# Optimization experiments

Hardware: AMD Instinct MI355X
Metric: run time of the kernel (lower is better)

Reference implementation:

```python
import jax, jax.numpy as jnp
import numpy as np

PARENTS = np.array([-1, 0, 1, 1, 1])
NECK_CHAIN = np.array([1, 0])  # neck joint (1) up to root (0)
B, V, F, J, S, E = 512, 5023, 9976, 5, 100, 50
L_STAT, L_DYN, L_FULL, N_BUCKET = 51, 17, 68, 79


def rodrigues(rvec):
    """Axis-angle [N,3] -> rotation matrices [N,3,3]."""
    angle = jnp.linalg.norm(rvec + 1e-8, axis=-1, keepdims=True)  # [N,1]
    axis = rvec / angle
    s = jnp.sin(angle)[..., None]
    c = jnp.cos(angle)[..., None]
    rx, ry, rz = axis[:, 0], axis[:, 1], axis[:, 2]
    z = jnp.zeros_like(rx)
    K = jnp.stack([z, -rz, ry, rz, z, -rx, -ry, rx, z], axis=-1).reshape(-1, 3, 3)
    I = jnp.eye(3, dtype=rvec.dtype)
    return I + s * K + (1.0 - c) * (K @ K)


def verts2lmk(vertices, faces, lmk_faces_idx, lmk_bary):
    lmk_faces = faces[lmk_faces_idx]                               # [B,L,3]
    lmk_verts = jax.vmap(lambda v, f: v[f])(vertices, lmk_faces)   # [B,L,3verts,3xyz]
    return jnp.einsum('blfc,blf->blc', lmk_verts, lmk_bary)


def setup_inputs() -> dict:
    key = jax.random.key(0)
    ks = jax.random.split(key, 16)
    shape_params = jax.random.normal(ks[0], (B, S), jnp.float32)
    expression_params = jax.random.normal(ks[1], (B, E), jnp.float32)
    pose_params = 0.2 * jax.random.normal(ks[2], (B, 6), jnp.float32)
    eye_pose_params = 0.1 * jax.random.normal(ks[3], (B, 6), jnp.float32)
    v_template = jax.random.normal(ks[4], (V, 3), jnp.float32) * 0.1
    shapedirs = jax.random.normal(ks[5], (V, 3, S + E), jnp.float32) * 0.01
    posedirs = jax.random.normal(ks[6], ((J - 1) * 9, V * 3), jnp.float32) * 0.01
    jr = jax.random.uniform(ks[7], (J, V), jnp.float32)
    J_regressor = jr / jnp.sum(jr, axis=1, keepdims=True)
    lbs_weights = jax.nn.softmax(jax.random.normal(ks[8], (V, J), jnp.float32), axis=-1)
    faces = jax.random.randint(ks[9], (F, 3), 0, V)
    lmk_faces_idx = jax.random.randint(ks[10], (L_STAT,), 0, F)
    lb = jax.random.uniform(ks[11], (L_STAT, 3), jnp.float32) + 1e-3
    lmk_bary_coords = lb / jnp.sum(lb, axis=-1, keepdims=True)
    dynamic_lmk_faces_idx = jax.random.randint(ks[12], (N_BUCKET, L_DYN), 0, F)
    db = jax.random.uniform(ks[13], (N_BUCKET, L_DYN, 3), jnp.float32) + 1e-3
    dynamic_lmk_bary_coords = db / jnp.sum(db, axis=-1, keepdims=True)
    full_lmk_faces_idx = jax.random.randint(ks[14], (L_FULL,), 0, F)
    fb = jax.random.uniform(ks[15], (L_FULL, 3), jnp.float32) + 1e-3
    full_lmk_bary_coords = fb / jnp.sum(fb, axis=-1, keepdims=True)
    return {
        'shape_params': shape_params, 'expression_params': expression_params,
        'pose_params': pose_params, 'eye_pose_params': eye_pose_params,
        'v_template': v_template, 'shapedirs': shapedirs, 'posedirs': posedirs,
        'J_regressor': J_regressor, 'lbs_weights': lbs_weights, 'faces': faces,
        'lmk_faces_idx': lmk_faces_idx, 'lmk_bary_coords': lmk_bary_coords,
        'dynamic_lmk_faces_idx': dynamic_lmk_faces_idx,
        'dynamic_lmk_bary_coords': dynamic_lmk_bary_coords,
        'full_lmk_faces_idx': full_lmk_faces_idx,
        'full_lmk_bary_coords': full_lmk_bary_coords,
    }


def reference(shape_params, expression_params, pose_params, eye_pose_params,
              v_template, shapedirs, posedirs, J_regressor, lbs_weights, faces,
              lmk_faces_idx, lmk_bary_coords, dynamic_lmk_faces_idx,
              dynamic_lmk_bary_coords, full_lmk_faces_idx, full_lmk_bary_coords):
    b = shape_params.shape[0]
    nv = v_template.shape[0]
    dt = shape_params.dtype
    betas = jnp.concatenate([shape_params, expression_params], axis=1)          # [B,150]
    neck = jnp.zeros((b, 3), dtype=dt)
    full_pose = jnp.concatenate(
        [pose_params[:, :3], neck, pose_params[:, 3:], eye_pose_params], axis=1)  # [B,15]
    # shape + expression blendshapes
    v_shaped = v_template[None] + jnp.einsum('bl,vcl->bvc', betas, shapedirs)   # [B,V,3]
    joints = jnp.einsum('jv,bvc->bjc', J_regressor, v_shaped)                   # [B,5,3]
    rot_mats = rodrigues(full_pose.reshape(-1, 3)).reshape(b, J, 3, 3)          # [B,5,3,3]
    I3 = jnp.eye(3, dtype=dt)
    pose_feature = (rot_mats[:, 1:] - I3).reshape(b, -1)                        # [B,36]
    v_posed = v_shaped + (pose_feature @ posedirs).reshape(b, nv, 3)
    # kinematic chain -> global joint transforms
    rel_J = joints.at[:, 1:].add(-joints[:, PARENTS[1:]])
    tm = jnp.zeros((b, J, 4, 4), dtype=dt)
    tm = tm.at[:, :, :3, :3].set(rot_mats).at[:, :, :3, 3].set(rel_J).at[:, :, 3, 3].set(1.0)
    chain = [tm[:, 0]]
    for i in range(1, J):
        chain.append(chain[PARENTS[i]] @ tm[:, i])
    A = jnp.stack(chain, axis=1)                                                # [B,5,4,4]
    Rj = jnp.einsum('bjmn,bjn->bjm', A[:, :, :3, :3], joints)
    A_rel = A.at[:, :, :3, 3].add(-Rj)
    # per-vertex skinning
    T = jnp.einsum('vj,bjmn->bvmn', lbs_weights, A_rel)                         # [B,V,4,4]
    vertices = jnp.einsum('bvmn,bvn->bvm', T[:, :, :3, :3], v_posed) + T[:, :, :3, 3]
    # dynamic contour landmark selection from neck kin-chain relative rotation
    aa = full_pose.reshape(b, J, 3)[:, NECK_CHAIN]                              # [B,2,3]
    rc = rodrigues(aa.reshape(-1, 3)).reshape(b, len(NECK_CHAIN), 3, 3)
    rel_rot = jnp.broadcast_to(I3, (b, 3, 3))
    for idx in range(len(NECK_CHAIN)):
        rel_rot = rc[:, idx] @ rel_rot
    sy = jnp.sqrt(rel_rot[:, 0, 0] ** 2 + rel_rot[:, 1, 0] ** 2)
    y_deg = jnp.arctan2(-rel_rot[:, 2, 0], sy) * (180.0 / np.pi)
    y_rot = jnp.round(jnp.minimum(y_deg, 39.0)).astype(jnp.int32)
    neg_mask = y_rot < 0
    big_neg = y_rot < -39
    neg_vals = jnp.where(big_neg, 78, 39 - y_rot)
    y_rot = jnp.where(neg_mask, neg_vals, y_rot)                                # [B] in [0,79)
    dyn_faces = dynamic_lmk_faces_idx[y_rot]                                    # [B,17]
    dyn_bary = dynamic_lmk_bary_coords[y_rot]                                   # [B,17,3]
    lf = jnp.concatenate([dyn_faces, jnp.broadcast_to(lmk_faces_idx[None], (b, lmk_faces_idx.shape[0]))], axis=1)
    lb = jnp.concatenate([dyn_bary, jnp.broadcast_to(lmk_bary_coords[None], (b,) + lmk_bary_coords.shape)], axis=1)
    landmarks2d = verts2lmk(vertices, faces, lf, lb)
    ff = jnp.broadcast_to(full_lmk_faces_idx[None], (b, full_lmk_faces_idx.shape[0]))
    fb = jnp.broadcast_to(full_lmk_bary_coords[None], (b,) + full_lmk_bary_coords.shape)
    landmarks3d = verts2lmk(vertices, faces, ff, fb)
    return (vertices, landmarks2d, landmarks3d)
```

## Files before the change

kernel.cpp:

```cpp
#include <hip/hip_runtime.h>
#include <cstddef>
#include <cstdint>

#define cB   512
#define cV   5023
#define cS   100
#define cE   50
#define cJ   5
#define cLD  17
#define cLF  68

#define cV3    15069
#define cNPAD  15072
#define cKPAD  192

#define OUT_V  ((size_t)cB * cV * 3)
#define OUT_L  ((size_t)cB * cLF * 3)

#define WS_BTN   ((size_t)0)
#define WS_ATM   (WS_BTN + (size_t)cNPAD * 96)
#define WS_JS    (WS_ATM + (size_t)cB * 96)
#define WS_AREL  (WS_JS + 2272)
#define WS_PF    (WS_AREL + (size_t)cB * 60)
#define WS_YROT  (WS_PF + (size_t)cB * 36)

typedef __attribute__((ext_vector_type(8))) short short8;
typedef __attribute__((ext_vector_type(4))) float f32x4;

__device__ __forceinline__ unsigned short f2bf(float x) {
  unsigned int u = __float_as_uint(x);
  u = (u + 0x7fffu + ((u >> 16) & 1u)) >> 16;
  return (unsigned short)u;
}

__device__ __forceinline__ void rodrigues9(float rx, float ry, float rz, float* R) {
  float a0 = rx + 1e-8f, a1 = ry + 1e-8f, a2 = rz + 1e-8f;
  float angle = sqrtf(a0 * a0 + a1 * a1 + a2 * a2);
  float inv = 1.0f / angle;
  float x = rx * inv, y = ry * inv, z = rz * inv;
  float s = sinf(angle), c = cosf(angle);
  float t = 1.0f - c;
  float xy = x * y, xz = x * z, yz = y * z;
  R[0] = 1.0f - t * (y * y + z * z);
  R[1] = -s * z + t * xy;
  R[2] =  s * y + t * xz;
  R[3] =  s * z + t * xy;
  R[4] = 1.0f - t * (x * x + z * z);
  R[5] = -s * x + t * yz;
  R[6] = -s * y + t * xz;
  R[7] =  s * x + t * yz;
  R[8] = 1.0f - t * (x * x + y * y);
}

__global__ void k_js(const float* __restrict__ jreg, const float* __restrict__ sd,
                     const float* __restrict__ vt, float* __restrict__ JS) {
  int t = threadIdx.x;
  if (t >= 453) return;
  int c = t / 151, l = t - c * 151;
  int v0 = blockIdx.x * 32;
  int v1 = v0 + 32; if (v1 > cV) v1 = cV;
  float acc[5] = {0.f, 0.f, 0.f, 0.f, 0.f};
#pragma unroll 8
  for (int v = v0; v < v1; ++v) {
    float x = (l < 150) ? sd[(size_t)(v * 3 + c) * 150 + l] : vt[v * 3 + c];
#pragma unroll
    for (int j = 0; j < 5; ++j)
      acc[j] = fmaf(jreg[j * cV + v], x, acc[j]);
  }
#pragma unroll
  for (int j = 0; j < 5; ++j)
    atomicAdd(&JS[(j * 3 + c) * 151 + l], acc[j]);
}

__global__ __launch_bounds__(256) void k_batch(
    const float* __restrict__ shp, const float* __restrict__ expr,
    const float* __restrict__ pose, const float* __restrict__ eyep,
    const float* __restrict__ JSg, float* __restrict__ Arel,
    float* __restrict__ pf, int* __restrict__ yrot) {
  __shared__ float js[2272];
  __shared__ float sb[64 * 153];
  const int t = threadIdx.x;
  const int b0 = blockIdx.x * 64;
  for (int i = t; i < 2265; i += 256) js[i] = JSg[i];
  for (int e = t; e < 6400; e += 256) {
    int bl = e / 100, l = e - bl * 100;
    sb[bl * 153 + l] = shp[(size_t)(b0 + bl) * 100 + l];
  }
  for (int e = t; e < 3200; e += 256) {
    int bl = e / 50, l = e - bl * 50;
    sb[bl * 153 + 100 + l] = expr[(size_t)(b0 + bl) * 50 + l];
  }
  __syncthreads();
  if (t >= 64) return;
  int b = b0 + t;
  float jnt[5][3];
#pragma unroll
  for (int j = 0; j < 5; ++j)
#pragma unroll
    for (int c = 0; c < 3; ++c)
      jnt[j][c] = js[(j * 3 + c) * 151 + 150];
  for (int l = 0; l < 150; ++l) {
    float beta = sb[t * 153 + l];
#pragma unroll
    for (int j = 0; j < 5; ++j)
#pragma unroll
      for (int c = 0; c < 3; ++c)
        jnt[j][c] = fmaf(beta, js[(j * 3 + c) * 151 + l], jnt[j][c]);
  }
  float fp[5][3];
  fp[0][0] = pose[b * 6 + 0]; fp[0][1] = pose[b * 6 + 1]; fp[0][2] = pose[b * 6 + 2];
  fp[1][0] = 0.f; fp[1][1] = 0.f; fp[1][2] = 0.f;
  fp[2][0] = pose[b * 6 + 3]; fp[2][1] = pose[b * 6 + 4]; fp[2][2] = pose[b * 6 + 5];
  fp[3][0] = eyep[b * 6 + 0]; fp[3][1] = eyep[b * 6 + 1]; fp[3][2] = eyep[b * 6 + 2];
  fp[4][0] = eyep[b * 6 + 3]; fp[4][1] = eyep[b * 6 + 4]; fp[4][2] = eyep[b * 6 + 5];
  float R[5][9];
#pragma unroll
  for (int j = 0; j < 5; ++j) rodrigues9(fp[j][0], fp[j][1], fp[j][2], R[j]);
#pragma unroll
  for (int j = 1; j < 5; ++j)
#pragma unroll
    for (int r = 0; r < 9; ++r) {
      float id = (r == 0 || r == 4 || r == 8) ? 1.f : 0.f;
      pf[b * 36 + (j - 1) * 9 + r] = R[j][r] - id;
    }
  float rel[5][3];
#pragma unroll
  for (int c = 0; c < 3; ++c) {
    rel[0][c] = jnt[0][c];
    rel[1][c] = jnt[1][c] - jnt[0][c];
    rel[2][c] = jnt[2][c] - jnt[1][c];
    rel[3][c] = jnt[3][c] - jnt[1][c];
    rel[4][c] = jnt[4][c] - jnt[1][c];
  }
  float GR[5][9], Gt[5][3];
#pragma unroll
  for (int r = 0; r < 9; ++r) GR[0][r] = R[0][r];
#pragma unroll
  for (int c = 0; c < 3; ++c) Gt[0][c] = rel[0][c];
  const int par[5] = {0, 0, 1, 1, 1};
#pragma unroll
  for (int j = 1; j < 5; ++j) {
    int p = par[j];
#pragma unroll
    for (int r = 0; r < 3; ++r) {
#pragma unroll
      for (int cc = 0; cc < 3; ++cc)
        GR[j][r * 3 + cc] = GR[p][r * 3 + 0] * R[j][0 + cc] +
                            GR[p][r * 3 + 1] * R[j][3 + cc] +
                            GR[p][r * 3 + 2] * R[j][6 + cc];
      Gt[j][r] = Gt[p][r] + GR[p][r * 3 + 0] * rel[j][0] +
                            GR[p][r * 3 + 1] * rel[j][1] +
                            GR[p][r * 3 + 2] * rel[j][2];
    }
  }
#pragma unroll
  for (int j = 0; j < 5; ++j)
#pragma unroll
    for (int r = 0; r < 3; ++r) {
      float tj = Gt[j][r] - (GR[j][r * 3 + 0] * jnt[j][0] +
                             GR[j][r * 3 + 1] * jnt[j][1] +
                             GR[j][r * 3 + 2] * jnt[j][2]);
      Arel[b * 60 + j * 12 + r * 4 + 0] = GR[j][r * 3 + 0];
      Arel[b * 60 + j * 12 + r * 4 + 1] = GR[j][r * 3 + 1];
      Arel[b * 60 + j * 12 + r * 4 + 2] = GR[j][r * 3 + 2];
      Arel[b * 60 + j * 12 + r * 4 + 3] = tj;
    }
  float Ra[9], Rb[9];
  rodrigues9(fp[1][0], fp[1][1], fp[1][2], Ra);
  rodrigues9(fp[0][0], fp[0][1], fp[0][2], Rb);
  float r00 = Rb[0] * Ra[0] + Rb[1] * Ra[3] + Rb[2] * Ra[6];
  float r10 = Rb[3] * Ra[0] + Rb[4] * Ra[3] + Rb[5] * Ra[6];
  float r20 = Rb[6] * Ra[0] + Rb[7] * Ra[3] + Rb[8] * Ra[6];
  float sy = sqrtf(r00 * r00 + r10 * r10);
  float ydeg = atan2f(-r20, sy) * 57.29577951308232f;
  int y = (int)rintf(fminf(ydeg, 39.0f));
  if (y < 0) y = (y < -39) ? 78 : (39 - y);
  yrot[b] = y;
}

#define QB ((size_t)cNPAD * 48)
__global__ void k_prep(const float* __restrict__ sd, const float* __restrict__ shp,
                       const float* __restrict__ expr, const float* __restrict__ pfm,
                       unsigned int* __restrict__ btn_u2, unsigned int* __restrict__ atm_u2) {
  size_t idx = (size_t)blockIdx.x * 256 + threadIdx.x;
  unsigned short o[4];
  if (idx < QB) {
    int n = (int)(idx / 48), kq = (int)(idx - (size_t)n * 48);
#pragma unroll
    for (int j = 0; j < 4; ++j) {
      int k = kq * 4 + j;
      float v = (n < cV3 && k < 150) ? sd[(size_t)n * 150 + k] : 0.f;
      o[j] = f2bf(v);
    }
    btn_u2[idx * 2 + 0] = (unsigned int)o[0] | ((unsigned int)o[1] << 16);
    btn_u2[idx * 2 + 1] = (unsigned int)o[2] | ((unsigned int)o[3] << 16);
  } else {
    size_t r = idx - QB;
    int m = (int)(r / 48), kq = (int)(r - (size_t)m * 48);
#pragma unroll
    for (int j = 0; j < 4; ++j) {
      int k = kq * 4 + j;
      float v;
      if (k < cS)            v = shp[m * cS + k];
      else if (k < 150)      v = expr[m * cE + (k - cS)];
      else if (k < 186)      v = pfm[m * 36 + (k - 150)];
      else                   v = 0.f;
      o[j] = f2bf(v);
    }
    atm_u2[r * 2 + 0] = (unsigned int)o[0] | ((unsigned int)o[1] << 16);
    atm_u2[r * 2 + 1] = (unsigned int)o[2] | ((unsigned int)o[3] << 16);
  }
}

__global__ void k_pdT(const float* __restrict__ pd, unsigned int* __restrict__ btn_u) {
  __shared__ unsigned short T[64 * 36];
  const int t = threadIdx.x;
  const int n0 = blockIdx.x * 64;
#pragma unroll
  for (int it = 0; it < 9; ++it) {
    int e = t + it * 256;
    int kk = e >> 6, ln = e & 63;
    int n = n0 + ln;
    float v = (n < cV3) ? pd[(size_t)kk * cV3 + n] : 0.f;
    T[ln * 36 + kk] = f2bf(v);
  }
  __syncthreads();
  for (int e = t; e < 64 * 18; e += 256) {
    int ln = e / 18, d = e - ln * 18;
    int n = n0 + ln;
    if (n < cV3) {
      unsigned int w = (unsigned int)T[ln * 36 + 2 * d] |
                       ((unsigned int)T[ln * 36 + 2 * d + 1] << 16);
      btn_u[(size_t)n * 96 + 75 + d] = w;
    }
  }
}

__global__ __launch_bounds__(256, 4) void k_main(
    const unsigned short* __restrict__ BTn, const unsigned short* __restrict__ ATm,
    const float* __restrict__ Arel, const float* __restrict__ vtempl,
    const float* __restrict__ lbw, float* __restrict__ out) {
  __shared__ __align__(16) unsigned short smem[19200];
  float* Pf = (float*)smem;

  const int t  = threadIdx.x;
  const int nb = blockIdx.x, mb = blockIdx.y;
  const int w = t >> 6, L = t & 63;
  const int wm = w >> 1, wn = w & 1;
  const int lr = L & 15, lq = L >> 4;

  const unsigned short* bsrc = BTn + (size_t)nb * 96 * 192;
  uint4 bst[9];
#pragma unroll
  for (int it = 0; it < 9; ++it)
    bst[it] = *(const uint4*)(bsrc + ((size_t)(t + it * 256)) * 8);

  const unsigned short* abase = ATm + ((size_t)mb * 64 + wm * 32 + lr) * 192 + lq * 8;
  short8 af[6][2];
#pragma unroll
  for (int ks = 0; ks < 6; ++ks)
#pragma unroll
    for (int mt = 0; mt < 2; ++mt)
      af[ks][mt] = *(const short8*)(abase + (size_t)mt * 16 * 192 + ks * 32);

#pragma unroll
  for (int it = 0; it < 9; ++it) {
    int e = t + it * 256;
    int row = e / 24, col = e - row * 24;
    *(uint4*)(smem + row * 200 + col * 8) = bst[it];
  }
  __syncthreads();

  f32x4 acc[2][3];
#pragma unroll
  for (int mt = 0; mt < 2; ++mt)
#pragma unroll
    for (int nt = 0; nt < 3; ++nt) acc[mt][nt] = (f32x4){0.f, 0.f, 0.f, 0.f};

#pragma unroll
  for (int ks = 0; ks < 6; ++ks) {
    const int ko = ks * 32 + lq * 8;
    short8 bf[3];
#pragma unroll
    for (int nt = 0; nt < 3; ++nt)
      bf[nt] = *(const short8*)(smem + (wn * 48 + nt * 16 + lr) * 200 + ko);
#pragma unroll
    for (int mt = 0; mt < 2; ++mt)
#pragma unroll
      for (int nt = 0; nt < 3; ++nt)
        acc[mt][nt] = __builtin_amdgcn_mfma_f32_16x16x32_bf16(af[ks][mt], bf[nt], acc[mt][nt], 0, 0, 0);
  }
  __syncthreads();

#pragma unroll
  for (int mt = 0; mt < 2; ++mt)
#pragma unroll
    for (int nt = 0; nt < 3; ++nt) {
      int m_base = wm * 32 + mt * 16 + lq * 4;
      int n_loc  = wn * 48 + nt * 16 + lr;
      *(f32x4*)(Pf + n_loc * 68 + m_base) = acc[mt][nt];
    }
  __syncthreads();

  const int v_loc = t & 31, bgrp = t >> 5;
  const int v = nb * 32 + v_loc;
  float wj[5], vtl[3];
  const bool vok = (v < cV);
#pragma unroll
  for (int j = 0; j < 5; ++j) wj[j] = vok ? lbw[v * 5 + j] : 0.f;
#pragma unroll
  for (int c = 0; c < 3; ++c) vtl[c] = vok ? vtempl[v * 3 + c] : 0.f;

#pragma unroll
  for (int i = 0; i < 8; ++i) {
    const int b_loc = bgrp * 8 + i;
    const float* q = Arel + ((size_t)mb * 64 + b_loc) * 60;
    float px = Pf[(v_loc * 3 + 0) * 68 + b_loc] + vtl[0];
    float py = Pf[(v_loc * 3 + 1) * 68 + b_loc] + vtl[1];
    float pz = Pf[(v_loc * 3 + 2) * 68 + b_loc] + vtl[2];
    float o0 = 0.f, o1 = 0.f, o2 = 0.f;
#pragma unroll
    for (int j = 0; j < 5; ++j) {
      f32x4 q0 = *(const f32x4*)(q + j * 12);
      f32x4 q1 = *(const f32x4*)(q + j * 12 + 4);
      f32x4 q2 = *(const f32x4*)(q + j * 12 + 8);
      float s0 = q0.x * px + q0.y * py + q0.z * pz + q0.w;
      float s1 = q1.x * px + q1.y * py + q1.z * pz + q1.w;
      float s2 = q2.x * px + q2.y * py + q2.z * pz + q2.w;
      o0 = fmaf(wj[j], s0, o0);
      o1 = fmaf(wj[j], s1, o1);
      o2 = fmaf(wj[j], s2, o2);
    }
    if (vok) {
      const int b = mb * 64 + b_loc;
      size_t off = ((size_t)b * cV + v) * 3;
      out[off + 0] = o0;
      out[off + 1] = o1;
      out[off + 2] = o2;
    }
  }
}

__global__ void k_lmk(const float* __restrict__ verts, const int* __restrict__ faces,
                      const int* __restrict__ lmkf, const float* __restrict__ lmkb,
                      const int* __restrict__ dynf, const float* __restrict__ dynb,
                      const int* __restrict__ fullf, const float* __restrict__ fullb,
                      const int* __restrict__ yrot, float* __restrict__ out) {
  int id = blockIdx.x * 256 + threadIdx.x;
  if (id >= cB * cLF * 2) return;
  int sel = id & 1;
  int r = id >> 1;
  int b = r / cLF, l = r - b * cLF;
  const float* vb = verts + (size_t)b * cV * 3;
  int f; float w0, w1, w2; size_t o;
  if (sel == 0) {
    if (l < cLD) {
      int yb = yrot[b];
      f = dynf[yb * cLD + l];
      const float* bp = dynb + ((size_t)yb * cLD + l) * 3;
      w0 = bp[0]; w1 = bp[1]; w2 = bp[2];
    } else {
      f = lmkf[l - cLD];
      const float* bp = lmkb + (size_t)(l - cLD) * 3;
      w0 = bp[0]; w1 = bp[1]; w2 = bp[2];
    }
    o = OUT_V + ((size_t)b * cLF + l) * 3;
  } else {
    f = fullf[l];
    const float* bp = fullb + (size_t)l * 3;
    w0 = bp[0]; w1 = bp[1]; w2 = bp[2];
    o = OUT_V + OUT_L + ((size_t)b * cLF + l) * 3;
  }
  int i0 = faces[f * 3 + 0] * 3, i1 = faces[f * 3 + 1] * 3, i2 = faces[f * 3 + 2] * 3;
  out[o + 0] = w0 * vb[i0 + 0] + w1 * vb[i1 + 0] + w2 * vb[i2 + 0];
  out[o + 1] = w0 * vb[i0 + 1] + w1 * vb[i1 + 1] + w2 * vb[i2 + 1];
  out[o + 2] = w0 * vb[i0 + 2] + w1 * vb[i1 + 2] + w2 * vb[i2 + 2];
}

extern "C" void kernel_launch(void* const* d_in, const int* in_sizes, int n_in,
                              void* d_out, int out_size, void* d_ws, size_t ws_size,
                              hipStream_t stream) {
  (void)in_sizes; (void)n_in; (void)out_size; (void)ws_size;
  const float* shp  = (const float*)d_in[0];
  const float* expr = (const float*)d_in[1];
  const float* pose = (const float*)d_in[2];
  const float* eyep = (const float*)d_in[3];
  const float* vt   = (const float*)d_in[4];
  const float* sd   = (const float*)d_in[5];
  const float* pd   = (const float*)d_in[6];
  const float* jreg = (const float*)d_in[7];
  const float* lbw  = (const float*)d_in[8];
  const int*   fcs  = (const int*)d_in[9];
  const int*   lmkf = (const int*)d_in[10];
  const float* lmkb = (const float*)d_in[11];
  const int*   dynf = (const int*)d_in[12];
  const float* dynb = (const float*)d_in[13];
  const int*   fullf= (const int*)d_in[14];
  const float* fullb= (const float*)d_in[15];
  float* out = (float*)d_out;
  float* ws  = (float*)d_ws;

  unsigned short* BTn = (unsigned short*)(ws + WS_BTN);
  unsigned short* ATm = (unsigned short*)(ws + WS_ATM);
  float* JS   = ws + WS_JS;
  float* Arel = ws + WS_AREL;
  float* pf   = ws + WS_PF;
  int*   yrot = (int*)(ws + WS_YROT);

  hipMemsetAsync(JS, 0, 2272 * sizeof(float), stream);
  k_js<<<157, 512, 0, stream>>>(jreg, sd, vt, JS);
  k_batch<<<8, 256, 0, stream>>>(shp, expr, pose, eyep, JS, Arel, pf, yrot);
  k_prep<<<2922, 256, 0, stream>>>(sd, shp, expr, pf,
                                   (unsigned int*)BTn, (unsigned int*)ATm);
  k_pdT<<<236, 256, 0, stream>>>(pd, (unsigned int*)BTn);
  k_main<<<dim3(157, 8), 256, 0, stream>>>(BTn, ATm, Arel, vt, lbw, out);
  k_lmk<<<272, 256, 0, stream>>>(out, fcs, lmkf, lmkb, dynf, dynb, fullf, fullb, yrot, out);
}
```

Before: 210.4 us.

## Replace joint-regressor atomics with partial-sum reduction and swizzle main GEMM block order

The joint-shape regression kernel now writes per-block partial sums into scratch space, which temporarily reuses the BTn region, and a new small kernel reduces them into a transposed layout. This removes the memset and the float atomics, and makes the result deterministic. k_batch reads the transposed table with vectorized float4 loads. k_main switches to a 1-D swizzled grid that groups eight vertex blocks per batch block for cache locality. It also loads its A fragments inside the k-loop instead of preloading them all, and drops the min-blocks-per-SM launch bound, which trades register pressure against load latency.

```diff
diff --git a/kernel.cpp b/kernel.cpp
--- a/kernel.cpp
+++ b/kernel.cpp
@@ -19,8 +19,8 @@
 
 #define WS_BTN   ((size_t)0)
 #define WS_ATM   (WS_BTN + (size_t)cNPAD * 96)
-#define WS_JS    (WS_ATM + (size_t)cB * 96)
-#define WS_AREL  (WS_JS + 2272)
+#define WS_JS2   (WS_ATM + (size_t)cB * 96)
+#define WS_AREL  (WS_JS2 + 2432)
 #define WS_PF    (WS_AREL + (size_t)cB * 60)
 #define WS_YROT  (WS_PF + (size_t)cB * 36)
 
@@ -53,7 +53,7 @@
 }
 
 __global__ void k_js(const float* __restrict__ jreg, const float* __restrict__ sd,
-                     const float* __restrict__ vt, float* __restrict__ JS) {
+                     const float* __restrict__ vt, float* __restrict__ JSpart) {
   int t = threadIdx.x;
   if (t >= 453) return;
   int c = t / 151, l = t - c * 151;
@@ -69,19 +69,30 @@
   }
 #pragma unroll
   for (int j = 0; j < 5; ++j)
-    atomicAdd(&JS[(j * 3 + c) * 151 + l], acc[j]);
+    JSpart[(size_t)blockIdx.x * 2272 + (j * 3 + c) * 151 + l] = acc[j];
+}
+
+__global__ void k_jsred(const float* __restrict__ JSpart, float* __restrict__ JS2) {
+  int e = blockIdx.x * 256 + threadIdx.x;
+  if (e >= 2265) return;
+  float s = 0.f;
+#pragma unroll 8
+  for (int p = 0; p < 157; ++p)
+    s += JSpart[(size_t)p * 2272 + e];
+  int jc = e / 151, l = e - jc * 151;
+  JS2[l * 16 + jc] = s;
 }
 
 __global__ __launch_bounds__(256) void k_batch(
     const float* __restrict__ shp, const float* __restrict__ expr,
     const float* __restrict__ pose, const float* __restrict__ eyep,
-    const float* __restrict__ JSg, float* __restrict__ Arel,
+    const float* __restrict__ JS2g, float* __restrict__ Arel,
     float* __restrict__ pf, int* __restrict__ yrot) {
-  __shared__ float js[2272];
+  __shared__ float js2[151 * 16];
   __shared__ float sb[64 * 153];
   const int t = threadIdx.x;
   const int b0 = blockIdx.x * 64;
-  for (int i = t; i < 2265; i += 256) js[i] = JSg[i];
+  for (int i = t; i < 151 * 16; i += 256) js2[i] = JS2g[i];
   for (int e = t; e < 6400; e += 256) {
     int bl = e / 100, l = e - bl * 100;
     sb[bl * 153 + l] = shp[(size_t)(b0 + bl) * 100 + l];
@@ -94,18 +105,34 @@
   if (t >= 64) return;
   int b = b0 + t;
   float jnt[5][3];
-#pragma unroll
-  for (int j = 0; j < 5; ++j)
-#pragma unroll
-    for (int c = 0; c < 3; ++c)
-      jnt[j][c] = js[(j * 3 + c) * 151 + 150];
+  {
+    const f32x4* J4 = (const f32x4*)(js2 + 150 * 16);
+    f32x4 A = J4[0], Bq = J4[1], Cq = J4[2], Dq = J4[3];
+    jnt[0][0] = A.x;  jnt[0][1] = A.y;  jnt[0][2] = A.z;
+    jnt[1][0] = A.w;  jnt[1][1] = Bq.x; jnt[1][2] = Bq.y;
+    jnt[2][0] = Bq.z; jnt[2][1] = Bq.w; jnt[2][2] = Cq.x;
+    jnt[3][0] = Cq.y; jnt[3][1] = Cq.z; jnt[3][2] = Cq.w;
+    jnt[4][0] = Dq.x; jnt[4][1] = Dq.y; jnt[4][2] = Dq.z;
+  }
   for (int l = 0; l < 150; ++l) {
+    const f32x4* J4 = (const f32x4*)(js2 + l * 16);
+    f32x4 A = J4[0], Bq = J4[1], Cq = J4[2], Dq = J4[3];
     float beta = sb[t * 153 + l];
-#pragma unroll
-    for (int j = 0; j < 5; ++j)
-#pragma unroll
-      for (int c = 0; c < 3; ++c)
-        jnt[j][c] = fmaf(beta, js[(j * 3 + c) * 151 + l], jnt[j][c]);
+    jnt[0][0] = fmaf(beta, A.x,  jnt[0][0]);
+    jnt[0][1] = fmaf(beta, A.y,  jnt[0][1]);
+    jnt[0][2] = fmaf(beta, A.z,  jnt[0][2]);
+    jnt[1][0] = fmaf(beta, A.w,  jnt[1][0]);
+    jnt[1][1] = fmaf(beta, Bq.x, jnt[1][1]);
+    jnt[1][2] = fmaf(beta, Bq.y, jnt[1][2]);
+    jnt[2][0] = fmaf(beta, Bq.z, jnt[2][0]);
+    jnt[2][1] = fmaf(beta, Bq.w, jnt[2][1]);
+    jnt[2][2] = fmaf(beta, Cq.x, jnt[2][2]);
+    jnt[3][0] = fmaf(beta, Cq.y, jnt[3][0]);
+    jnt[3][1] = fmaf(beta, Cq.z, jnt[3][1]);
+    jnt[3][2] = fmaf(beta, Cq.w, jnt[3][2]);
+    jnt[4][0] = fmaf(beta, Dq.x, jnt[4][0]);
+    jnt[4][1] = fmaf(beta, Dq.y, jnt[4][1]);
+    jnt[4][2] = fmaf(beta, Dq.z, jnt[4][2]);
   }
   float fp[5][3];
   fp[0][0] = pose[b * 6 + 0]; fp[0][1] = pose[b * 6 + 1]; fp[0][2] = pose[b * 6 + 2];
@@ -236,15 +263,20 @@
   }
 }
 
-__global__ __launch_bounds__(256, 4) void k_main(
+__global__ __launch_bounds__(256) void k_main(
     const unsigned short* __restrict__ BTn, const unsigned short* __restrict__ ATm,
     const float* __restrict__ Arel, const float* __restrict__ vtempl,
     const float* __restrict__ lbw, float* __restrict__ out) {
   __shared__ __align__(16) unsigned short smem[19200];
   float* Pf = (float*)smem;
 
-  const int t  = threadIdx.x;
-  const int nb = blockIdx.x, mb = blockIdx.y;
+  const int bid = blockIdx.x;
+  const int r8 = bid & 7, q = bid >> 3;
+  const int mb = q & 7, nbh = q >> 3;
+  const int nb = (nbh << 3) | r8;
+  if (nb >= 157) return;
+
+  const int t = threadIdx.x;
   const int w = t >> 6, L = t & 63;
   const int wm = w >> 1, wn = w & 1;
   const int lr = L & 15, lq = L >> 4;
@@ -254,15 +286,6 @@
 #pragma unroll
   for (int it = 0; it < 9; ++it)
     bst[it] = *(const uint4*)(bsrc + ((size_t)(t + it * 256)) * 8);
-
-  const unsigned short* abase = ATm + ((size_t)mb * 64 + wm * 32 + lr) * 192 + lq * 8;
-  short8 af[6][2];
-#pragma unroll
-  for (int ks = 0; ks < 6; ++ks)
-#pragma unroll
-    for (int mt = 0; mt < 2; ++mt)
-      af[ks][mt] = *(const short8*)(abase + (size_t)mt * 16 * 192 + ks * 32);
-
 #pragma unroll
   for (int it = 0; it < 9; ++it) {
     int e = t + it * 256;
@@ -277,18 +300,21 @@
 #pragma unroll
     for (int nt = 0; nt < 3; ++nt) acc[mt][nt] = (f32x4){0.f, 0.f, 0.f, 0.f};
 
+  const unsigned short* abase = ATm + ((size_t)mb * 64 + wm * 32 + lr) * 192 + lq * 8;
 #pragma unroll
   for (int ks = 0; ks < 6; ++ks) {
+    short8 af0 = *(const short8*)(abase + ks * 32);
+    short8 af1 = *(const short8*)(abase + 16 * 192 + ks * 32);
     const int ko = ks * 32 + lq * 8;
     short8 bf[3];
 #pragma unroll
     for (int nt = 0; nt < 3; ++nt)
       bf[nt] = *(const short8*)(smem + (wn * 48 + nt * 16 + lr) * 200 + ko);
 #pragma unroll
-    for (int mt = 0; mt < 2; ++mt)
-#pragma unroll
-      for (int nt = 0; nt < 3; ++nt)
-        acc[mt][nt] = __builtin_amdgcn_mfma_f32_16x16x32_bf16(af[ks][mt], bf[nt], acc[mt][nt], 0, 0, 0);
+    for (int nt = 0; nt < 3; ++nt) {
+      acc[0][nt] = __builtin_amdgcn_mfma_f32_16x16x32_bf16(af0, bf[nt], acc[0][nt], 0, 0, 0);
+      acc[1][nt] = __builtin_amdgcn_mfma_f32_16x16x32_bf16(af1, bf[nt], acc[1][nt], 0, 0, 0);
+    }
   }
   __syncthreads();
 
@@ -314,16 +340,16 @@
 #pragma unroll
   for (int i = 0; i < 8; ++i) {
     const int b_loc = bgrp * 8 + i;
-    const float* q = Arel + ((size_t)mb * 64 + b_loc) * 60;
+    const float* qb = Arel + ((size_t)mb * 64 + b_loc) * 60;
     float px = Pf[(v_loc * 3 + 0) * 68 + b_loc] + vtl[0];
     float py = Pf[(v_loc * 3 + 1) * 68 + b_loc] + vtl[1];
     float pz = Pf[(v_loc * 3 + 2) * 68 + b_loc] + vtl[2];
     float o0 = 0.f, o1 = 0.f, o2 = 0.f;
 #pragma unroll
     for (int j = 0; j < 5; ++j) {
-      f32x4 q0 = *(const f32x4*)(q + j * 12);
-      f32x4 q1 = *(const f32x4*)(q + j * 12 + 4);
-      f32x4 q2 = *(const f32x4*)(q + j * 12 + 8);
+      f32x4 q0 = *(const f32x4*)(qb + j * 12);
+      f32x4 q1 = *(const f32x4*)(qb + j * 12 + 4);
+      f32x4 q2 = *(const f32x4*)(qb + j * 12 + 8);
       float s0 = q0.x * px + q0.y * py + q0.z * pz + q0.w;
       float s1 = q1.x * px + q1.y * py + q1.z * pz + q1.w;
       float s2 = q2.x * px + q2.y * py + q2.z * pz + q2.w;
@@ -402,17 +428,18 @@
 
   unsigned short* BTn = (unsigned short*)(ws + WS_BTN);
   unsigned short* ATm = (unsigned short*)(ws + WS_ATM);
-  float* JS   = ws + WS_JS;
+  float* JSpart = ws + WS_BTN;
+  float* JS2  = ws + WS_JS2;
   float* Arel = ws + WS_AREL;
   float* pf   = ws + WS_PF;
   int*   yrot = (int*)(ws + WS_YROT);
 
-  hipMemsetAsync(JS, 0, 2272 * sizeof(float), stream);
-  k_js<<<157, 512, 0, stream>>>(jreg, sd, vt, JS);
-  k_batch<<<8, 256, 0, stream>>>(shp, expr, pose, eyep, JS, Arel, pf, yrot);
+  k_js<<<157, 512, 0, stream>>>(jreg, sd, vt, JSpart);
+  k_jsred<<<9, 256, 0, stream>>>(JSpart, JS2);
+  k_batch<<<8, 256, 0, stream>>>(shp, expr, pose, eyep, JS2, Arel, pf, yrot);
   k_prep<<<2922, 256, 0, stream>>>(sd, shp, expr, pf,
                                    (unsigned int*)BTn, (unsigned int*)ATm);
   k_pdT<<<236, 256, 0, stream>>>(pd, (unsigned int*)BTn);
-  k_main<<<dim3(157, 8), 256, 0, stream>>>(BTn, ATm, Arel, vt, lbw, out);
+  k_main<<<1280, 256, 0, stream>>>(BTn, ATm, Arel, vt, lbw, out);
   k_lmk<<<272, 256, 0, stream>>>(out, fcs, lmkf, lmkb, dynf, dynb, fullf, fullb, yrot, out);
 }
```

Result: faster. 186.5 us (-11.4%).
